# Kernel tuning notes

Hardware: AMD Instinct MI355X
Metric: run time of the kernel (lower is better)

The kernel has to match this reference:

```python
import jax, jax.numpy as jnp
import numpy as np

B = 16384      # batch
CNUM = 2048    # codebook entries
K = 8          # topk
D = 10         # emb_dim
M = 50         # meta_dim
UID = 1000000
IID = 1000000
TAU = 10.0


def setup_inputs() -> dict:
    key = jax.random.key(0)
    ks = jax.random.split(key, 14)
    uid_col = jax.random.randint(ks[0], (B, 1), 0, UID, dtype=jnp.int64)
    iid_col = jax.random.randint(ks[1], (B, 1), 0, IID + 1, dtype=jnp.int64)
    x = jnp.concatenate([uid_col, iid_col], axis=1)
    return {
        "x": x,
        "gumbel_u_src": jax.random.uniform(ks[2], (B, CNUM), dtype=jnp.float32),
        "gumbel_u_tgt": jax.random.uniform(ks[3], (B, CNUM), dtype=jnp.float32),
        "src_uid_table": jax.random.normal(ks[4], (UID, D), dtype=jnp.float32),
        "tgt_uid_table": jax.random.normal(ks[5], (UID, D), dtype=jnp.float32),
        "tgt_iid_table": jax.random.normal(ks[6], (IID + 1, D), dtype=jnp.float32),
        "C": jax.random.normal(ks[7], (CNUM, M), dtype=jnp.float32) * 0.01,
        "w1": jax.random.normal(ks[8], (D, M), dtype=jnp.float32) * 0.01,
        "w2": jax.random.normal(ks[9], (M, D), dtype=jnp.float32) * 0.01,
        "mw1": jax.random.normal(ks[10], (D + M, 50), dtype=jnp.float32) * 0.1,
        "mb1": jnp.zeros((50,), dtype=jnp.float32),
        "mw2": jax.random.normal(ks[11], (50, D * D), dtype=jnp.float32) * 0.1,
        "mb2": jnp.zeros((D * D,), dtype=jnp.float32),
    }


def _gumbel_route(u_emb, C, w1, u_noise):
    # u_emb: [B, D] -> logits s_u: [B, CNUM]
    s = jnp.einsum('bm,cm->bc', u_emb @ w1, C)
    g = -jnp.log(-jnp.log(u_noise + 1e-20) + 1e-20)  # gumbel noise
    gw = jax.nn.softmax((s + g) / TAU, axis=-1)       # F.gumbel_softmax, hard=False
    tw, ti = jax.lax.top_k(gw, K)                     # [B, K]
    c_u = C[ti]                                       # [B, K, M] codebook gather
    return tw, ti, c_u


def reference(x, gumbel_u_src, gumbel_u_tgt, src_uid_table, tgt_uid_table,
              tgt_iid_table, C, w1, w2, mw1, mb1, mw2, mb2):
    # ---- stage == 'test_meta' ----
    # target-side interest embedding ('test_interst' path)
    tuid = tgt_uid_table[x[:, 0]]                      # [B, D]
    tw_t, _, c_t = _gumbel_route(tuid, C, w1, gumbel_u_tgt)
    tuid_ins = ((c_t * tw_t[..., None]).sum(axis=1)) @ w2   # [B, D]
    # source-side routing ('test_meta' path of InterstEmbedding)
    uid = src_uid_table[x[:, 0]]                       # [B, D]
    tw_s, _, c_s = _gumbel_route(uid, C, w1, gumbel_u_src)
    src_fea = jnp.broadcast_to(uid[:, None, :], (uid.shape[0], K, D))  # [B, K, D]
    inp = jnp.concatenate([c_s, src_fea], axis=-1)     # [B, K, M+D] = [B, K, 60]
    h = jax.nn.relu(inp @ mw1 + mb1)                   # [B, K, 50]
    mapping = (h @ mw2 + mb2).reshape(-1, K, D, D)     # per-sample hypernet weights
    src_emb = jnp.einsum('bkd,bkde->bke', src_fea, mapping)  # [B, K, D]
    pre_emb = (src_emb * tw_s[..., None]).sum(axis=1)  # [B, D]
    fin_emb = tuid_ins + pre_emb                       # [B, D]
    iid_emb = tgt_iid_table[x[:, 1]]                   # [B, D]
    return jnp.sum(fin_emb * iid_emb, axis=-1)         # [B]
```

## Files before the change

kernel.cpp:

```cpp
#include <hip/hip_runtime.h>
#include <hip/hip_bf16.h>


#define BROWS 16384
#define CNUM  2048
#define KSEL  8
#define DIMD  10
#define MDIM  50
#define RPB   16
#define RTPB  32
#define CH    128
#define NCH   (CNUM/CH)
#define TAUI  0.1f
#define T24   24

#define OFF_C0   0
#define OFF_C1   4096
#define OFF_PF   8192
#define OFF_T24  9856
#define OFF_T24L 10624
#define OFF_TS   11392
#define OFF_TW   11456
#define OFF_TI   11712
#define OFF_UD   11968
#define SMEM_W   12160

typedef float    f32x4 __attribute__((ext_vector_type(4)));
typedef _Float16 half8 __attribute__((ext_vector_type(8)));
typedef float    flt2  __attribute__((ext_vector_type(2)));
typedef unsigned int u32;

__device__ __forceinline__ u32 pkrtz(float a, float b) {
    auto h = __builtin_amdgcn_cvt_pkrtz(a, b);
    union { decltype(h) v; u32 u; } c; c.v = h; return c.u;
}
__device__ __forceinline__ float gnoise(float u) {
    return -__logf(-__logf(u + 1e-20f) + 1e-20f);
}

__global__ void cvtC(const float* __restrict__ Cm, u32* __restrict__ C16) {
    const int j = blockIdx.x * 256 + threadIdx.x;
    const int cand = j >> 5, w = j & 31, k = 2 * w;
    const float a = (k < MDIM)     ? Cm[cand*MDIM + k]     : 0.f;
    const float b = (k + 1 < MDIM) ? Cm[cand*MDIM + k + 1] : 0.f;
    C16[j] = pkrtz(a, b);
}

template<bool PRE>
__global__ __launch_bounds__(256, 3)
void mf_fused(const int* __restrict__ x32,
              const float* __restrict__ gsrc,
              const float* __restrict__ gtgt,
              const float* __restrict__ suid,
              const float* __restrict__ tuid,
              const float* __restrict__ tiid,
              const float* __restrict__ Cm,
              const float* __restrict__ w1,
              const float* __restrict__ w2,
              const float* __restrict__ mw1,
              const float* __restrict__ mb1,
              const float* __restrict__ mw2,
              const float* __restrict__ mb2,
              const u32* __restrict__ C16,
              float* __restrict__ out)
{
    __shared__ __align__(16) float smem[SMEM_W];
    __shared__ int sFlag;
    u32*   W    = (u32*)smem;
    float* sPf  = smem + OFF_PF;
    u32*   T24u = (u32*)(smem + OFF_T24);
    float* T24l = smem + OFF_T24L;

    const int tid  = threadIdx.x;
    const int row0 = blockIdx.x * RPB;

    if (tid == 0) sFlag = 1;
    __syncthreads();
    if (tid < 128) { if (x32[2*tid+1] != 0) atomicAnd(&sFlag, 0); }
    __syncthreads();
    const int is64 = sFlag;

    for (int t = tid; t < RTPB*52; t += 256) {
        const int rt = t / 52, mm = t - rt*52;
        float v = 0.f;
        if (mm < MDIM) {
            const int r = row0 + (rt >> 1);
            const int uidx = is64 ? x32[4*r] : x32[2*r];
            const float* tab = (rt & 1) ? suid : tuid;
            #pragma unroll
            for (int d = 0; d < DIMD; ++d) v += tab[uidx*DIMD + d] * w1[d*MDIM + mm];
        }
        sPf[t] = v;
    }

    u32 sw[16];
    const int xorv = ((tid >> 3) & 7) << 2;
    auto issue = [&](int ch) {
        if (PRE) {
            const uint4* src = (const uint4*)C16;
            #pragma unroll
            for (int i = 0; i < 4; ++i) {
                uint4 t4 = src[ch*1024 + i*256 + tid];
                sw[i*4+0] = t4.x; sw[i*4+1] = t4.y; sw[i*4+2] = t4.z; sw[i*4+3] = t4.w;
            }
        } else {
            #pragma unroll
            for (int i = 0; i < 4; ++i)
                #pragma unroll
                for (int w2i = 0; w2i < 4; ++w2i) {
                    const int cand = ch*CH + (tid >> 3) + i*32;
                    const int widx = (tid*4 + w2i) & 31, k = 2*widx;
                    const float a = (k < MDIM)     ? Cm[cand*MDIM + k]     : 0.f;
                    const float b = (k + 1 < MDIM) ? Cm[cand*MDIM + k + 1] : 0.f;
                    sw[i*4 + w2i] = pkrtz(a, b);
                }
        }
    };
    auto commit = [&](int buf) {
        u32* B = W + buf*4096;
        #pragma unroll
        for (int i = 0; i < 4; ++i)
            *(uint4*)&B[(tid*4 + i*1024) ^ xorv] =
                make_uint4(sw[i*4], sw[i*4+1], sw[i*4+2], sw[i*4+3]);
    };

    issue(0); commit(0);
    __syncthreads();

    const int lane = tid & 63, wv = tid >> 6;
    const int lr = lane & 15, lk = lane >> 4;
    const int g = wv & 1, h = wv >> 1;
    const int rt = g*16 + lr;
    const int xorr = (lr & 7) << 2;
    const float* up = ((lr & 1) ? gsrc : gtgt) + (size_t)(row0 + g*8 + (lr >> 1)) * CNUM;

    half8 b0, b1;
    {
        union { u32 u[4]; half8 v; } c0, c1;
        #pragma unroll
        for (int jj = 0; jj < 4; ++jj) {
            const int k0 = lk*8 + jj*2;
            c0.u[jj] = pkrtz(sPf[rt*52 + k0], sPf[rt*52 + k0 + 1]);
            const int k1 = 32 + lk*8 + jj*2;
            const float e0 = (k1     < 52) ? sPf[rt*52 + k1]     : 0.f;
            const float e1 = (k1 + 1 < 52) ? sPf[rt*52 + k1 + 1] : 0.f;
            c1.u[jj] = pkrtz(e0, e1);
        }
        b0 = c0.v; b1 = c1.v;
    }

    float ts = 0.f;
    float q0=-3.4e38f,q1=-3.4e38f,q2=-3.4e38f,q3=-3.4e38f,
          q4=-3.4e38f,q5=-3.4e38f,q6=-3.4e38f,q7=-3.4e38f;

    for (int ch = 0; ch < NCH; ++ch) {
        if (ch + 1 < NCH) issue(ch + 1);
        const u32* Bf = W + (ch & 1)*4096;
        #pragma unroll
        for (int nt = 0; nt < 4; ++nt) {
            const int cl = h*64 + nt*16;
            const int wb = (cl + lr) * 32;
            const half8 a0 = *(const half8*)&Bf[(wb +      lk*4) ^ xorr];
            const half8 a1 = *(const half8*)&Bf[(wb + 16 + lk*4) ^ xorr];
            f32x4 acc = {0.f, 0.f, 0.f, 0.f};
            acc = __builtin_amdgcn_mfma_f32_16x16x32_f16(a0, b0, acc, 0, 0, 0);
            acc = __builtin_amdgcn_mfma_f32_16x16x32_f16(a1, b1, acc, 0, 0, 0);
            const f32x4 u4 = *(const f32x4*)(up + ch*CH + cl + lk*4);
            const int cg = ch*CH + cl + lk*4;
            #pragma unroll
            for (int r4 = 0; r4 < 4; ++r4) {
                const float l = (acc[r4] + gnoise(u4[r4])) * TAUI;
                ts += __expf(l);
                const float xs = __uint_as_float(
                    (__float_as_uint(l) & 0xFFFFF800u) | (u32)(cg + r4));
                q0 = fmaxf(q0, fminf(q1, xs));
                q1 = fmaxf(q1, fminf(q2, xs));
                q2 = fmaxf(q2, fminf(q3, xs));
                q3 = fmaxf(q3, fminf(q4, xs));
                q4 = fmaxf(q4, fminf(q5, xs));
                q5 = fmaxf(q5, fminf(q6, xs));
                q6 = fmaxf(q6, fminf(q7, xs));
                q7 = fmaxf(q7, xs);
            }
        }
        if (ch + 1 < NCH) commit((ch + 1) & 1);
        __syncthreads();
    }

    {
        float tss = ts;
        tss += __shfl_xor(tss, 16); tss += __shfl_xor(tss, 32);
        if (lk == 0) smem[OFF_TS + rt*2 + h] = tss;
        #pragma unroll
        for (int k = 0; k < 12; ++k) {
            float gm = fmaxf(q7, __shfl_xor(q7, 16));
            gm = fmaxf(gm, __shfl_xor(gm, 32));
            if (q7 == gm) {
                T24u[rt*T24 + h*12 + k] = __float_as_uint(q7);
                q7=q6; q6=q5; q5=q4; q4=q3; q3=q2; q2=q1; q1=q0; q0=-3.4e38f;
            }
        }
    }
    __syncthreads();

    for (int e = tid; e < RTPB*T24; e += 256) {
        const int ert = e / T24;
        const int idx = (int)(T24u[e] & 2047u);
        const float* pf = sPf + ert*52;
        const float* cr = Cm + idx*MDIM;
        float s = 0.f;
        #pragma unroll
        for (int k2 = 0; k2 < 25; ++k2) {
            flt2 c = *(const flt2*)(cr + k2*2);
            s += pf[2*k2] * c.x + pf[2*k2+1] * c.y;
        }
        const int r = row0 + (ert >> 1);
        const float u = ((ert & 1) ? gsrc : gtgt)[(size_t)r*CNUM + idx];
        T24l[e] = (s + gnoise(u)) * TAUI;
    }
    __syncthreads();

    if (tid < RTPB) {
        const int rrt = tid;
        const float inv = 1.0f / (smem[OFF_TS + rrt*2] + smem[OFF_TS + rrt*2 + 1]);
        float lv[T24]; int iv[T24];
        #pragma unroll
        for (int j = 0; j < T24; ++j) {
            lv[j] = T24l[rrt*T24 + j];
            iv[j] = (int)(T24u[rrt*T24 + j] & 2047u);
        }
        u32 used = 0;
        #pragma unroll
        for (int k = 0; k < KSEL; ++k) {
            float bl = -3.4e38f; int bi = 1 << 30; int bj = 0;
            #pragma unroll
            for (int j = 0; j < T24; ++j) {
                const bool ok = !((used >> j) & 1);
                if (ok && (lv[j] > bl || (lv[j] == bl && iv[j] < bi))) { bl = lv[j]; bi = iv[j]; bj = j; }
            }
            used |= 1u << bj;
            smem[OFF_TW + rrt*KSEL + k] = __expf(bl) * inv;
            ((int*)smem)[OFF_TI + rrt*KSEL + k] = bi;
        }
    }
    __syncthreads();

    float* sH    = smem;
    float* sQ    = smem + 832;
    float* sUd   = smem + OFF_UD;
    float* sTopW = smem + OFF_TW;
    int*   sTopI = (int*)smem + OFF_TI;

    const int gg = tid >> 4, lg = tid & 15;
    const int row = row0 + gg;
    const int rt_t = gg*2, rt_s = gg*2 + 1;
    const int uidx = is64 ? x32[4*row]     : x32[2*row];
    const int iidx = is64 ? x32[4*row + 2] : x32[2*row + 1];

    if (lg < DIMD) sUd[gg*12 + lg] = suid[uidx*DIMD + lg];
    __syncthreads();

    for (int t = lg; t < MDIM*DIMD; t += 16) {
        const int j = t / DIMD, e = t - j*DIMD;
        float q = 0.f;
        #pragma unroll
        for (int d = 0; d < DIMD; ++d) q += sUd[gg*12 + d] * mw2[j*(DIMD*DIMD) + d*DIMD + e];
        sQ[gg*500 + t] = q;
    }
    for (int mm = lg; mm < MDIM; mm += 16) {
        float v = 0.f;
        #pragma unroll
        for (int k = 0; k < KSEL; ++k)
            v += sTopW[rt_t*KSEL + k] * Cm[sTopI[rt_t*KSEL + k]*MDIM + mm];
        sH[gg*52 + mm] = v;
    }
    __syncthreads();

    float acc_e = 0.f, be = 0.f;
    if (lg < DIMD) {
        for (int m2 = 0; m2 < MDIM; ++m2) acc_e += sH[gg*52 + m2] * w2[m2*DIMD + lg];
        #pragma unroll
        for (int d = 0; d < DIMD; ++d) be += sUd[gg*12 + d] * mb2[d*DIMD + lg];
    }
    __syncthreads();

    for (int k = 0; k < KSEL; ++k) {
        const int   ik = sTopI[rt_s*KSEL + k];
        const float tw = sTopW[rt_s*KSEL + k];
        for (int j = lg; j < MDIM; j += 16) {
            float hh = mb1[j];
            const float* crow = Cm + ik*MDIM;
            for (int t2 = 0; t2 < MDIM; ++t2) hh += crow[t2] * mw1[t2*MDIM + j];
            #pragma unroll
            for (int d = 0; d < DIMD; ++d) hh += sUd[gg*12 + d] * mw1[(MDIM + d)*MDIM + j];
            sH[gg*52 + j] = fmaxf(hh, 0.f);
        }
        __syncthreads();
        if (lg < DIMD) {
            float se = be;
            for (int j = 0; j < MDIM; ++j) se += sH[gg*52 + j] * sQ[gg*500 + j*DIMD + lg];
            acc_e += tw * se;
        }
        __syncthreads();
    }

    float o = 0.f;
    if (lg < DIMD) o = acc_e * tiid[iidx*DIMD + lg];
    #pragma unroll
    for (int k = 8; k >= 1; k >>= 1) o += __shfl_xor(o, k, 16);
    if (lg == 0) out[row] = o;
}

extern "C" void kernel_launch(void* const* d_in, const int* in_sizes, int n_in,
                              void* d_out, int out_size, void* d_ws, size_t ws_size,
                              hipStream_t stream) {
    (void)in_sizes; (void)n_in; (void)out_size;
    const int*   x32  = (const int*)d_in[0];
    const float* gsrc = (const float*)d_in[1];
    const float* gtgt = (const float*)d_in[2];
    const float* suid = (const float*)d_in[3];
    const float* tuid = (const float*)d_in[4];
    const float* tiid = (const float*)d_in[5];
    const float* Cm   = (const float*)d_in[6];
    const float* w1   = (const float*)d_in[7];
    const float* w2   = (const float*)d_in[8];
    const float* mw1  = (const float*)d_in[9];
    const float* mb1  = (const float*)d_in[10];
    const float* mw2  = (const float*)d_in[11];
    const float* mb2  = (const float*)d_in[12];
    u32* C16 = (u32*)d_ws;

    if (ws_size >= 262144) {
        hipLaunchKernelGGL(cvtC, dim3(256), dim3(256), 0, stream, Cm, C16);
        hipLaunchKernelGGL(mf_fused<true>, dim3(BROWS/RPB), dim3(256), 0, stream,
                           x32, gsrc, gtgt, suid, tuid, tiid, Cm, w1, w2, mw1, mb1, mw2, mb2,
                           C16, (float*)d_out);
    } else {
        hipLaunchKernelGGL(mf_fused<false>, dim3(BROWS/RPB), dim3(256), 0, stream,
                           x32, gsrc, gtgt, suid, tuid, tiid, Cm, w1, w2, mw1, mb1, mw2, mb2,
                           C16, (float*)d_out);
    }
}
```

Baseline: 290.6 us.

## Load codebook MFMA fragments directly from global, dropping LDS double buffering

The codebook is no longer staged chunk by chunk into a double-buffered, XOR-swizzled LDS area. Each wave now reads its f16 A fragments straight from the pre-converted global codebook, which should stay cache-resident, inside a single 64-tile loop. This removes the per-chunk __syncthreads barriers and about 8K words of shared memory, and the launch bounds are raised from 3 to 4 blocks per SM to use the freed LDS. In exchange, every wave re-fetches codebook data from L2/global instead of sharing one LDS copy per block, which adds cache traffic and load latency on the critical path.

```diff
diff --git a/kernel.cpp b/kernel.cpp
--- a/kernel.cpp
+++ b/kernel.cpp
@@ -9,21 +9,17 @@
 #define MDIM  50
 #define RPB   16
 #define RTPB  32
-#define CH    128
-#define NCH   (CNUM/CH)
 #define TAUI  0.1f
 #define T24   24
 
-#define OFF_C0   0
-#define OFF_C1   4096
-#define OFF_PF   8192
-#define OFF_T24  9856
-#define OFF_T24L 10624
-#define OFF_TS   11392
-#define OFF_TW   11456
-#define OFF_TI   11712
-#define OFF_UD   11968
-#define SMEM_W   12160
+#define OFF_PF   0
+#define OFF_T24  1664
+#define OFF_T24L 2432
+#define OFF_TS   3200
+#define OFF_TW   8832
+#define OFF_TI   9088
+#define OFF_UD   9344
+#define SMEM_W   9536
 
 typedef float    f32x4 __attribute__((ext_vector_type(4)));
 typedef _Float16 half8 __attribute__((ext_vector_type(8)));
@@ -47,7 +43,7 @@
 }
 
 template<bool PRE>
-__global__ __launch_bounds__(256, 3)
+__global__ __launch_bounds__(256, 4)
 void mf_fused(const int* __restrict__ x32,
               const float* __restrict__ gsrc,
               const float* __restrict__ gtgt,
@@ -66,7 +62,6 @@
 {
     __shared__ __align__(16) float smem[SMEM_W];
     __shared__ int sFlag;
-    u32*   W    = (u32*)smem;
     float* sPf  = smem + OFF_PF;
     u32*   T24u = (u32*)(smem + OFF_T24);
     float* T24l = smem + OFF_T24L;
@@ -92,46 +87,12 @@
         }
         sPf[t] = v;
     }
-
-    u32 sw[16];
-    const int xorv = ((tid >> 3) & 7) << 2;
-    auto issue = [&](int ch) {
-        if (PRE) {
-            const uint4* src = (const uint4*)C16;
-            #pragma unroll
-            for (int i = 0; i < 4; ++i) {
-                uint4 t4 = src[ch*1024 + i*256 + tid];
-                sw[i*4+0] = t4.x; sw[i*4+1] = t4.y; sw[i*4+2] = t4.z; sw[i*4+3] = t4.w;
-            }
-        } else {
-            #pragma unroll
-            for (int i = 0; i < 4; ++i)
-                #pragma unroll
-                for (int w2i = 0; w2i < 4; ++w2i) {
-                    const int cand = ch*CH + (tid >> 3) + i*32;
-                    const int widx = (tid*4 + w2i) & 31, k = 2*widx;
-                    const float a = (k < MDIM)     ? Cm[cand*MDIM + k]     : 0.f;
-                    const float b = (k + 1 < MDIM) ? Cm[cand*MDIM + k + 1] : 0.f;
-                    sw[i*4 + w2i] = pkrtz(a, b);
-                }
-        }
-    };
-    auto commit = [&](int buf) {
-        u32* B = W + buf*4096;
-        #pragma unroll
-        for (int i = 0; i < 4; ++i)
-            *(uint4*)&B[(tid*4 + i*1024) ^ xorv] =
-                make_uint4(sw[i*4], sw[i*4+1], sw[i*4+2], sw[i*4+3]);
-    };
-
-    issue(0); commit(0);
     __syncthreads();
 
     const int lane = tid & 63, wv = tid >> 6;
     const int lr = lane & 15, lk = lane >> 4;
     const int g = wv & 1, h = wv >> 1;
     const int rt = g*16 + lr;
-    const int xorr = (lr & 7) << 2;
     const float* up = ((lr & 1) ? gsrc : gtgt) + (size_t)(row0 + g*8 + (lr >> 1)) * CNUM;
 
     half8 b0, b1;
@@ -153,38 +114,48 @@
     float q0=-3.4e38f,q1=-3.4e38f,q2=-3.4e38f,q3=-3.4e38f,
           q4=-3.4e38f,q5=-3.4e38f,q6=-3.4e38f,q7=-3.4e38f;
 
-    for (int ch = 0; ch < NCH; ++ch) {
-        if (ch + 1 < NCH) issue(ch + 1);
-        const u32* Bf = W + (ch & 1)*4096;
-        #pragma unroll
-        for (int nt = 0; nt < 4; ++nt) {
-            const int cl = h*64 + nt*16;
-            const int wb = (cl + lr) * 32;
-            const half8 a0 = *(const half8*)&Bf[(wb +      lk*4) ^ xorr];
-            const half8 a1 = *(const half8*)&Bf[(wb + 16 + lk*4) ^ xorr];
-            f32x4 acc = {0.f, 0.f, 0.f, 0.f};
-            acc = __builtin_amdgcn_mfma_f32_16x16x32_f16(a0, b0, acc, 0, 0, 0);
-            acc = __builtin_amdgcn_mfma_f32_16x16x32_f16(a1, b1, acc, 0, 0, 0);
-            const f32x4 u4 = *(const f32x4*)(up + ch*CH + cl + lk*4);
-            const int cg = ch*CH + cl + lk*4;
+    #pragma unroll 4
+    for (int ti = 0; ti < 64; ++ti) {
+        const int cb = ((ti >> 2) << 7) + h*64 + ((ti & 3) << 4);
+        half8 a0, a1;
+        if (PRE) {
+            const u32* cr = C16 + (size_t)(cb + lr)*32 + lk*4;
+            a0 = *(const half8*)cr;
+            a1 = *(const half8*)(cr + 16);
+        } else {
+            const float* cr = Cm + (size_t)(cb + lr)*MDIM;
+            union { u32 u[4]; half8 v; } c0, c1;
             #pragma unroll
-            for (int r4 = 0; r4 < 4; ++r4) {
-                const float l = (acc[r4] + gnoise(u4[r4])) * TAUI;
-                ts += __expf(l);
-                const float xs = __uint_as_float(
-                    (__float_as_uint(l) & 0xFFFFF800u) | (u32)(cg + r4));
-                q0 = fmaxf(q0, fminf(q1, xs));
-                q1 = fmaxf(q1, fminf(q2, xs));
-                q2 = fmaxf(q2, fminf(q3, xs));
-                q3 = fmaxf(q3, fminf(q4, xs));
-                q4 = fmaxf(q4, fminf(q5, xs));
-                q5 = fmaxf(q5, fminf(q6, xs));
-                q6 = fmaxf(q6, fminf(q7, xs));
-                q7 = fmaxf(q7, xs);
+            for (int jj = 0; jj < 4; ++jj) {
+                const int k0 = lk*8 + jj*2;
+                c0.u[jj] = pkrtz(cr[k0], cr[k0+1]);
+                const int k1 = 32 + lk*8 + jj*2;
+                const float e0 = (k1     < MDIM) ? cr[k1]     : 0.f;
+                const float e1 = (k1 + 1 < MDIM) ? cr[k1+1] : 0.f;
+                c1.u[jj] = pkrtz(e0, e1);
             }
-        }
-        if (ch + 1 < NCH) commit((ch + 1) & 1);
-        __syncthreads();
+            a0 = c0.v; a1 = c1.v;
+        }
+        f32x4 acc = {0.f, 0.f, 0.f, 0.f};
+        acc = __builtin_amdgcn_mfma_f32_16x16x32_f16(a0, b0, acc, 0, 0, 0);
+        acc = __builtin_amdgcn_mfma_f32_16x16x32_f16(a1, b1, acc, 0, 0, 0);
+        const f32x4 u4 = *(const f32x4*)(up + cb + lk*4);
+        const int cg = cb + lk*4;
+        #pragma unroll
+        for (int r4 = 0; r4 < 4; ++r4) {
+            const float l = (acc[r4] + gnoise(u4[r4])) * TAUI;
+            ts += __expf(l);
+            const float xs = __uint_as_float(
+                (__float_as_uint(l) & 0xFFFFF800u) | (u32)(cg + r4));
+            q0 = fmaxf(q0, fminf(q1, xs));
+            q1 = fmaxf(q1, fminf(q2, xs));
+            q2 = fmaxf(q2, fminf(q3, xs));
+            q3 = fmaxf(q3, fminf(q4, xs));
+            q4 = fmaxf(q4, fminf(q5, xs));
+            q5 = fmaxf(q5, fminf(q6, xs));
+            q6 = fmaxf(q6, fminf(q7, xs));
+            q7 = fmaxf(q7, xs);
+        }
     }
 
     {
```

Measured after the change: 282.5 us. -2.8%, faster.
